# Kernel tuning notes

Hardware: AMD Instinct MI355X
Metric: run time of the kernel (lower is better)

## Reference

```python
import jax, jax.numpy as jnp
import numpy as np

B, T, N = 256, 512, 256
START, STOP = 254, 255


def setup_inputs() -> dict:
    key = jax.random.key(0)
    k1, k2, k3 = jax.random.split(key, 3)
    inputs = jax.random.normal(k1, (B, T, N), dtype=jnp.float32)
    transitions = jax.random.normal(k2, (N, N), dtype=jnp.float32)
    # sentinel rows/cols as in __init__
    transitions = transitions.at[START, :].set(-10000.0).at[:, STOP].set(-10000.0)
    tags = jax.random.randint(k3, (B, T), 0, N, dtype=jnp.int32)
    mask = jnp.ones((B, T), dtype=jnp.int32)
    return {"inputs": inputs, "transitions": transitions, "tags": tags, "mask": mask}


def _input_likelihood(inputs, transitions, fmask):
    # alpha[b, tag]: log-sum over paths ending at tag
    alpha0 = transitions[:, START][None, :] + inputs[:, 0, :]

    def step(alpha, xs):
        emit, m = xs  # emit: (B, N), m: (B,)
        # inner[b, next, prev] = alpha[b, prev] + (emit[b, next] + trans[next, prev]) * mask[b, i-1]
        inner = alpha[:, None, :] + (emit[:, :, None] + transitions[None, :, :]) * m[:, None, None]
        return jax.nn.logsumexp(inner, axis=-1), None

    xs = (jnp.swapaxes(inputs[:, 1:, :], 0, 1), jnp.swapaxes(fmask[:, :-1], 0, 1))
    alpha, _ = jax.lax.scan(step, alpha0, xs)
    stops = alpha + transitions[STOP][None, :]
    return jax.nn.logsumexp(stops, axis=-1)  # (B,)


def _joint_likelihood(inputs, transitions, tags, fmask):
    score = transitions[tags[:, 0], START]  # (B,)
    # transitions[next, prev] * mask[:, i+1], summed over steps
    trans_sc = transitions[tags[:, 1:], tags[:, :-1]] * fmask[:, 1:]
    # inputs[b, i, prev_tag] * mask[:, i]
    emit_sc = jnp.take_along_axis(inputs[:, :-1, :], tags[:, :-1, None], axis=2)[..., 0] * fmask[:, :-1]
    score = score + trans_sc.sum(axis=-1) + emit_sc.sum(axis=-1)
    last_idx = (fmask.sum(axis=-1) - 1.0).astype(jnp.int32)  # (B,)
    last_tags = jnp.take_along_axis(tags, last_idx[:, None], axis=1)[:, 0]
    last_input = jnp.take_along_axis(inputs[:, -1, :], last_tags[:, None], axis=1)[:, 0]
    return score + transitions[STOP, last_tags] + last_input * fmask[:, -1]


def reference(inputs, transitions, tags, mask):
    fmask = mask.astype(jnp.float32)
    log_denominator = _input_likelihood(inputs, transitions, fmask)
    log_numerator = _joint_likelihood(inputs, transitions, tags, fmask)
    return jnp.sum(log_numerator - log_denominator)
```

## Files before the change

### kernel.cpp

```cpp
#include <hip/hip_runtime.h>
#include <hip/hip_bf16.h>
#include <stdint.h>

#define B_    256
#define T_    512
#define N_    256
#define START_ 254
#define STOP_  255
#define GCOLS 16
#define NF    16
#define ND    32
#define LOG2E 1.4426950408889634f
#define LN2   0.6931471805599453f

#define WSB_OFF 65536
#define WCF_OFF 131072
#define WCB_OFF 131328

typedef __attribute__((ext_vector_type(4))) float floatx4;
typedef __attribute__((ext_vector_type(4))) unsigned int uintx4;
typedef __attribute__((ext_vector_type(8))) int v8i;

template<bool X> struct BC { static constexpr bool value = X; };

__device__ __forceinline__ void lds_barrier() {
    asm volatile("s_waitcnt lgkmcnt(0)\n\ts_barrier" ::: "memory");
}

__device__ __forceinline__ int pk_fp8x4(float a, float b, float c, float d) {
    int r = __builtin_amdgcn_cvt_pk_fp8_f32(a, b, 0, false);
    return __builtin_amdgcn_cvt_pk_fp8_f32(c, d, r, true);
}
__device__ __forceinline__ int pk_bf8x4(float a, float b, float c, float d) {
    int r = __builtin_amdgcn_cvt_pk_bf8_f32(a, b, 0, false);
    return __builtin_amdgcn_cvt_pk_bf8_f32(c, d, r, true);
}

struct DenomShared {
    alignas(16) char  V[2][4096];
    alignas(16) float mbuf[GCOLS * 36];
    alignas(16) float sbuf[GCOLS * 20];
    int flag;
};

template<bool ISF>
__device__ __forceinline__ void denom_path(
    DenomShared& sh, const float* __restrict__ inputs,
    const float* __restrict__ trans, const int* __restrict__ mask,
    float* __restrict__ ws, int blkLocal)
{
    const int tid = threadIdx.x;
    const int w = tid >> 6;
    const int l = tid & 63;
    const int q = l >> 4;
    const int b = l & 15;
    const int bg = blkLocal * GCOLS + b;
    const int j0 = 32 * w + 4 * q;
    const int S = ISF ? 256 : 255;
    const int scl = 0x7F7F7F7F;

    auto EIDX = [](int s) { return ISF ? s : (511 - s); };
    auto MIDX = [](int s) { return ISF ? (s - 1) : (511 - s); };

    int wa[2];
    #pragma unroll
    for (int mt = 0; mt < 2; ++mt)
        wa[mt] = ((((2 * w + mt) >> 3) * 2 + mt) << 10)
               + ((w & 3) << 8) + (b << 4) + (q << 2);
    const int rbase = l << 4;

    v8i afrag[2][2];
    #pragma unroll
    for (int mt = 0; mt < 2; ++mt) {
        const int row = 32 * w + 16 * mt + b;
        #pragma unroll
        for (int c = 0; c < 2; ++c) {
            v8i a;
            #pragma unroll
            for (int g8 = 0; g8 < 8; ++g8) {
                float e[4];
                if (ISF) {
                    floatx4 t = *(const floatx4*)(trans + row * N_ + c * 128 + q * 32 + 4 * g8);
                    #pragma unroll
                    for (int ii = 0; ii < 4; ++ii)
                        e[ii] = __builtin_amdgcn_exp2f(t[ii] * LOG2E);
                } else {
                    #pragma unroll
                    for (int ii = 0; ii < 4; ++ii) {
                        const int k = c * 128 + q * 32 + 4 * g8 + ii;
                        e[ii] = __builtin_amdgcn_exp2f(trans[k * N_ + row] * LOG2E);
                    }
                }
                a[g8] = pk_fp8x4(e[0], e[1], e[2], e[3]);
            }
            afrag[mt][c] = a;
        }
    }

    {
        const int* mrow = mask + blkLocal * GCOLS * T_;
        bool hd = false;
        #pragma unroll
        for (int i = 0; i < GCOLS * T_ / 512; ++i)
            hd |= (mrow[tid + 512 * i] == 0);
        if (tid == 0) sh.flag = 0;
        __syncthreads();
        if (__any(hd) && l == 0) atomicOr(&sh.flag, 1);
        __syncthreads();
    }
    const bool anyDead = (sh.flag != 0);

    const float* emitp = inputs + (size_t)bg * T_ * N_;
    const int*   maskp = mask + bg * T_;
    float C = 0.f;
    float u[2][4];

    if (ISF) {
        #pragma unroll
        for (int mt = 0; mt < 2; ++mt) {
            floatx4 em = *(const floatx4*)(emitp + j0 + 16 * mt);
            #pragma unroll
            for (int r = 0; r < 4; ++r) {
                const int j = j0 + 16 * mt + r;
                u[mt][r] = __builtin_amdgcn_exp2f((trans[j * N_ + START_] + em[r]) * LOG2E);
            }
        }
    } else {
        #pragma unroll
        for (int mt = 0; mt < 2; ++mt) {
            floatx4 st = *(const floatx4*)(trans + STOP_ * N_ + j0 + 16 * mt);
            #pragma unroll
            for (int r = 0; r < 4; ++r)
                u[mt][r] = __builtin_amdgcn_exp2f(st[r] * LOG2E);
        }
    }
    {
        float mx = u[0][0], sm = 0.f;
        #pragma unroll
        for (int mt = 0; mt < 2; ++mt)
            #pragma unroll
            for (int r = 0; r < 4; ++r) { mx = fmaxf(mx, u[mt][r]); sm += u[mt][r]; }
        sh.mbuf[b * 36 + w * 4 + q] = mx;
        sm += __shfl_xor(sm, 32, 64);
        if (l < 32) sh.sbuf[b * 20 + w * 2 + q] = sm;

        float xpi[2][4] = {{1.f,1.f,1.f,1.f},{1.f,1.f,1.f,1.f}};
        if (!ISF) {
            #pragma unroll
            for (int mt = 0; mt < 2; ++mt) {
                floatx4 e = *(const floatx4*)(emitp + (size_t)511 * N_ + j0 + 16 * mt);
                #pragma unroll
                for (int r = 0; r < 4; ++r)
                    xpi[mt][r] = __builtin_amdgcn_exp2f(e[r] * LOG2E);
            }
        }
        #pragma unroll
        for (int mt = 0; mt < 2; ++mt)
            *(int*)(sh.V[0] + wa[mt]) =
                pk_bf8x4(u[mt][0] * xpi[mt][0], u[mt][1] * xpi[mt][1],
                         u[mt][2] * xpi[mt][2], u[mt][3] * xpi[mt][3]);
    }

    auto run = [&](auto fastc) {
        constexpr bool FAST = decltype(fastc)::value;
        floatx4 ebuf[2][2];
        float   mrot[2] = {1.f, 1.f};
        ebuf[0][0] = *(const floatx4*)(emitp + (size_t)EIDX(1) * N_ + j0);
        ebuf[0][1] = *(const floatx4*)(emitp + (size_t)EIDX(1) * N_ + j0 + 16);
        ebuf[1][0] = *(const floatx4*)(emitp + (size_t)EIDX(2) * N_ + j0);
        ebuf[1][1] = *(const floatx4*)(emitp + (size_t)EIDX(2) * N_ + j0 + 16);
        if (!FAST) {
            mrot[0] = (float)maskp[MIDX(1)];
            mrot[1] = (float)maskp[MIDX(2)];
        }
        lds_barrier();

        auto body = [&](int s, int pr, int cur) {
            const int sp = (s + 2 <= S) ? s + 2 : S;
            floatx4 eC0 = *(const floatx4*)(emitp + (size_t)EIDX(sp) * N_ + j0);
            floatx4 eC1 = *(const floatx4*)(emitp + (size_t)EIDX(sp) * N_ + j0 + 16);
            float mC = 1.f;
            if (!FAST) mC = (float)maskp[MIDX(sp)];

            const char* vb = sh.V[pr];
            v8i bfrag[2];
            #pragma unroll
            for (int c = 0; c < 2; ++c) {
                uintx4 r0 = *(const uintx4*)(vb + (c << 11) + rbase);
                uintx4 r1 = *(const uintx4*)(vb + (c << 11) + 1024 + rbase);
                v8i bf;
                bf[0] = r0[0]; bf[1] = r0[1]; bf[2] = r0[2]; bf[3] = r0[3];
                bf[4] = r1[0]; bf[5] = r1[1]; bf[6] = r1[2]; bf[7] = r1[3];
                bfrag[c] = bf;
            }

            const float* mb = &sh.mbuf[b * 36];
            float cmax;
            {
                floatx4 mm[8];
                #pragma unroll
                for (int i = 0; i < 8; ++i) mm[i] = *(const floatx4*)(mb + 4 * i);
                floatx4 mv = mm[0];
                #pragma unroll
                for (int i = 1; i < 8; ++i)
                    #pragma unroll
                    for (int r = 0; r < 4; ++r) mv[r] = fmaxf(mv[r], mm[i][r]);
                cmax = fmaxf(fmaxf(mv[0], mv[1]), fmaxf(mv[2], mv[3]));
            }
            const uint32_t cb = __builtin_bit_cast(uint32_t, cmax);
            const int eb = (int)((cb >> 23) & 0xFFu);
            const float rs = __builtin_bit_cast(float, (uint32_t)(249 - eb) << 23);
            const float dCf = (float)(122 - eb);

            float xpv[2][4];
            #pragma unroll
            for (int r = 0; r < 4; ++r) {
                if (ISF) {
                    xpv[0][r] = __builtin_amdgcn_exp2f(fmaf(ebuf[cur][0][r], LOG2E, dCf));
                    xpv[1][r] = __builtin_amdgcn_exp2f(fmaf(ebuf[cur][1][r], LOG2E, dCf));
                } else {
                    xpv[0][r] = __builtin_amdgcn_exp2f(ebuf[cur][0][r] * LOG2E);
                    xpv[1][r] = __builtin_amdgcn_exp2f(ebuf[cur][1][r] * LOG2E);
                }
            }

            floatx4 a0 = {0.f,0.f,0.f,0.f}, a1 = {0.f,0.f,0.f,0.f};
            a0 = __builtin_amdgcn_mfma_scale_f32_16x16x128_f8f6f4(
                     afrag[0][0], bfrag[0], a0, 0, 1, 0, scl, 0, scl);
            a1 = __builtin_amdgcn_mfma_scale_f32_16x16x128_f8f6f4(
                     afrag[1][0], bfrag[0], a1, 0, 1, 0, scl, 0, scl);
            a0 = __builtin_amdgcn_mfma_scale_f32_16x16x128_f8f6f4(
                     afrag[0][1], bfrag[1], a0, 0, 1, 0, scl, 0, scl);
            a1 = __builtin_amdgcn_mfma_scale_f32_16x16x128_f8f6f4(
                     afrag[1][1], bfrag[1], a1, 0, 1, 0, scl, 0, scl);

            if (FAST) {
                #pragma unroll
                for (int r = 0; r < 4; ++r) {
                    if (ISF) {
                        u[0][r] = a0[r] * xpv[0][r];
                        u[1][r] = a1[r] * xpv[1][r];
                    } else {
                        u[0][r] = a0[r] * rs;
                        u[1][r] = a1[r] * rs;
                    }
                }
            } else {
                const bool live = (mrot[cur] != 0.f);
                float csv = 0.f;
                if (__any(!live)) {
                    const float* sb = &sh.sbuf[b * 20];
                    floatx4 s0 = *(const floatx4*)sb,       s1 = *(const floatx4*)(sb + 4);
                    floatx4 s2 = *(const floatx4*)(sb + 8), s3 = *(const floatx4*)(sb + 12);
                    csv = ((((s0[0] + s0[1]) + (s0[2] + s0[3])) +
                            ((s1[0] + s1[1]) + (s1[2] + s1[3]))) +
                           (((s2[0] + s2[1]) + (s2[2] + s2[3])) +
                            ((s3[0] + s3[1]) + (s3[2] + s3[3])))) * rs;
                }
                #pragma unroll
                for (int r = 0; r < 4; ++r) {
                    if (ISF) {
                        u[0][r] = live ? a0[r] * xpv[0][r] : csv;
                        u[1][r] = live ? a1[r] * xpv[1][r] : csv;
                    } else {
                        u[0][r] = live ? a0[r] * rs : csv;
                        u[1][r] = live ? a1[r] * rs : csv;
                    }
                }
            }
            C += (float)(eb - 122);

            {
                float mx = fmaxf(fmaxf(fmaxf(u[0][0], u[0][1]), fmaxf(u[0][2], u[0][3])),
                                 fmaxf(fmaxf(u[1][0], u[1][1]), fmaxf(u[1][2], u[1][3])));
                sh.mbuf[b * 36 + w * 4 + q] = mx;
                if (!FAST) {
                    float sm = ((u[0][0] + u[0][1]) + (u[0][2] + u[0][3]))
                             + ((u[1][0] + u[1][1]) + (u[1][2] + u[1][3]));
                    sm += __shfl_xor(sm, 32, 64);
                    if (l < 32) sh.sbuf[b * 20 + w * 2 + q] = sm;
                }
            }
            #pragma unroll
            for (int mt = 0; mt < 2; ++mt) {
                *(int*)(sh.V[pr ^ 1] + wa[mt]) = ISF
                    ? pk_bf8x4(u[mt][0], u[mt][1], u[mt][2], u[mt][3])
                    : pk_bf8x4(u[mt][0] * xpv[mt][0], u[mt][1] * xpv[mt][1],
                               u[mt][2] * xpv[mt][2], u[mt][3] * xpv[mt][3]);
            }
            lds_barrier();
            ebuf[cur][0] = eC0; ebuf[cur][1] = eC1;
            if (!FAST) mrot[cur] = mC;
        };

        #pragma unroll 1
        for (int g = 0; g < 127; ++g) {
            body(2 * g + 1, 0, 0);
            body(2 * g + 2, 1, 1);
        }
        if (ISF) { body(255, 0, 0); body(256, 1, 1); }
        else     { body(255, 0, 0); }
    };

    if (anyDead) run(BC<false>{});
    else         run(BC<true>{});

    float* wsV = ws + (ISF ? 0 : WSB_OFF);
    #pragma unroll
    for (int mt = 0; mt < 2; ++mt) {
        floatx4 vv = {u[mt][0], u[mt][1], u[mt][2], u[mt][3]};
        *(floatx4*)&wsV[(size_t)bg * N_ + j0 + 16 * mt] = vv;
    }
    if (tid < 16) {
        float* wsC = ws + (ISF ? WCF_OFF : WCB_OFF);
        wsC[blkLocal * GCOLS + tid] = C;
    }
}

__global__ __launch_bounds__(512, 2) void crf_main(
    const float* __restrict__ inputs, const float* __restrict__ trans,
    const int* __restrict__ tags, const int* __restrict__ mask,
    float* __restrict__ out, float* __restrict__ ws)
{
    __shared__ DenomShared sh;

    if (blockIdx.x >= ND) {
        float* nred = sh.sbuf;
        int*   nredi = (int*)(sh.sbuf + 8);
        const int bb = blockIdx.x - ND;
        const int t  = threadIdx.x;
        const int tg = tags[bb * T_ + t];
        const float fm = (float)mask[bb * T_ + t];
        float part = 0.f;
        if (t >= 1)      part += trans[tg * N_ + tags[bb * T_ + t - 1]] * fm;
        if (t <= T_ - 2) part += inputs[((size_t)bb * T_ + t) * N_ + tg] * fm;
        int ms = mask[bb * T_ + t];
        #pragma unroll
        for (int off = 1; off < 64; off <<= 1) {
            part += __shfl_xor(part, off, 64);
            ms   += __shfl_xor(ms, off, 64);
        }
        if ((t & 63) == 0) { nred[t >> 6] = part; nredi[t >> 6] = ms; }
        __syncthreads();
        if (t == 0) {
            float tot = 0.f; int mtot = 0;
            for (int i = 0; i < 8; ++i) { tot += nred[i]; mtot += nredi[i]; }
            tot += trans[tags[bb * T_] * N_ + START_];
            const int last = mtot - 1;
            const int lt = tags[bb * T_ + last];
            tot += trans[STOP_ * N_ + lt]
                 + inputs[((size_t)bb * T_ + (T_ - 1)) * N_ + lt]
                   * (float)mask[bb * T_ + T_ - 1];
            atomicAdd(out, tot);
        }
        return;
    }

    if (blockIdx.x < NF) denom_path<true>(sh, inputs, trans, mask, ws, blockIdx.x);
    else                 denom_path<false>(sh, inputs, trans, mask, ws, blockIdx.x - NF);
}

__global__ __launch_bounds__(256) void crf_combine(
    const float* __restrict__ ws, float* __restrict__ out)
{
    __shared__ float red[4];
    const int bb = blockIdx.x;
    const int t = threadIdx.x;
    float p = ws[(size_t)bb * N_ + t] * ws[WSB_OFF + (size_t)bb * N_ + t];
    #pragma unroll
    for (int off = 1; off < 64; off <<= 1) p += __shfl_xor(p, off, 64);
    if ((t & 63) == 0) red[t >> 6] = p;
    __syncthreads();
    if (t == 0) {
        const float tot = red[0] + red[1] + red[2] + red[3];
        const float denom = (ws[WCF_OFF + bb] + ws[WCB_OFF + bb]
                             + __builtin_amdgcn_logf(tot)) * LN2;
        atomicAdd(out, -denom);
    }
}

extern "C" void kernel_launch(void* const* d_in, const int* in_sizes, int n_in,
                              void* d_out, int out_size, void* d_ws, size_t ws_size,
                              hipStream_t stream) {
    const float* inputs = (const float*)d_in[0];
    const float* trans  = (const float*)d_in[1];
    const int*   tags   = (const int*)d_in[2];
    const int*   mask   = (const int*)d_in[3];
    float* out = (float*)d_out;
    float* ws  = (float*)d_ws;
    hipMemsetAsync(out, 0, sizeof(float), stream);
    crf_main<<<dim3(ND + B_), dim3(512), 0, stream>>>(inputs, trans, tags, mask, out, ws);
    crf_combine<<<dim3(B_), dim3(256), 0, stream>>>(ws, out);
}
```

Before: 341.0 us.

## Streamline serial CRF recurrence step: pointer-stepped prefetch, shuffle max, deferred exp

Reworks the per-timestep body of the forward/backward CRF recurrence. The running-max reduction now uses wave shuffles, so each step reads 8 floats from LDS instead of 32. Emission exponentials are computed one step ahead through a three-deep register rotation, and pointers are incremented rather than recomputing indices. The normalization exponent is accumulated as an integer and the forward scale is applied by multiplication instead of inside exp2. The numerator no longer uses one atomic per batch row; it goes to workspace, and the combine kernel handles 16 rows per block, which cuts atomics and blocks. The cost is more register pressure from the extra prefetch stage.

New measurement: 338.1 us. About the same (-0.9%).

```diff
diff --git a/kernel.cpp b/kernel.cpp
--- a/kernel.cpp
+++ b/kernel.cpp
@@ -16,6 +16,7 @@
 #define WSB_OFF 65536
 #define WCF_OFF 131072
 #define WCB_OFF 131328
+#define WNUM_OFF 131584
 
 typedef __attribute__((ext_vector_type(4))) float floatx4;
 typedef __attribute__((ext_vector_type(4))) unsigned int uintx4;
@@ -26,6 +27,9 @@
 __device__ __forceinline__ void lds_barrier() {
     asm volatile("s_waitcnt lgkmcnt(0)\n\ts_barrier" ::: "memory");
 }
+__device__ __forceinline__ float fmax3(float a, float b, float c) {
+    return fmaxf(fmaxf(a, b), c);
+}
 
 __device__ __forceinline__ int pk_fp8x4(float a, float b, float c, float d) {
     int r = __builtin_amdgcn_cvt_pk_fp8_f32(a, b, 0, false);
@@ -38,7 +42,7 @@
 
 struct DenomShared {
     alignas(16) char  V[2][4096];
-    alignas(16) float mbuf[GCOLS * 36];
+    alignas(16) float mbuf[GCOLS * 12];
     alignas(16) float sbuf[GCOLS * 20];
     int flag;
 };
@@ -112,7 +116,7 @@
 
     const float* emitp = inputs + (size_t)bg * T_ * N_;
     const int*   maskp = mask + bg * T_;
-    float C = 0.f;
+    int   Ci = 0;
     float u[2][4];
 
     if (ISF) {
@@ -135,12 +139,16 @@
         }
     }
     {
-        float mx = u[0][0], sm = 0.f;
+        float mx = fmaxf(fmax3(u[0][0], u[0][1], u[0][2]),
+                         fmax3(u[0][3], u[1][0], fmax3(u[1][1], u[1][2], u[1][3])));
+        float sm = 0.f;
         #pragma unroll
         for (int mt = 0; mt < 2; ++mt)
             #pragma unroll
-            for (int r = 0; r < 4; ++r) { mx = fmaxf(mx, u[mt][r]); sm += u[mt][r]; }
-        sh.mbuf[b * 36 + w * 4 + q] = mx;
+            for (int r = 0; r < 4; ++r) sm += u[mt][r];
+        mx = fmaxf(mx, __shfl_xor(mx, 16, 64));
+        mx = fmaxf(mx, __shfl_xor(mx, 32, 64));
+        if (l < 16) sh.mbuf[b * 12 + w] = mx;
         sm += __shfl_xor(sm, 32, 64);
         if (l < 32) sh.sbuf[b * 20 + w * 2 + q] = sm;
 
@@ -163,83 +171,94 @@
 
     auto run = [&](auto fastc) {
         constexpr bool FAST = decltype(fastc)::value;
-        floatx4 ebuf[2][2];
-        float   mrot[2] = {1.f, 1.f};
-        ebuf[0][0] = *(const floatx4*)(emitp + (size_t)EIDX(1) * N_ + j0);
-        ebuf[0][1] = *(const floatx4*)(emitp + (size_t)EIDX(1) * N_ + j0 + 16);
-        ebuf[1][0] = *(const floatx4*)(emitp + (size_t)EIDX(2) * N_ + j0);
-        ebuf[1][1] = *(const floatx4*)(emitp + (size_t)EIDX(2) * N_ + j0 + 16);
+        const long estep = ISF ? (long)N_ : -(long)N_;
+        const int  mstep = ISF ? 1 : -1;
+
+        floatx4 xc0, xc1;
+        floatx4 rbA0, rbA1;
+        floatx4 rbB0, rbB1;
+        const float* pe = emitp + (size_t)EIDX(1) * N_ + j0;
+        {
+            floatx4 e0 = *(const floatx4*)pe;
+            floatx4 e1 = *(const floatx4*)(pe + 16);
+            pe += estep;
+            rbA0 = *(const floatx4*)pe;
+            rbA1 = *(const floatx4*)(pe + 16);
+            pe += estep;
+            rbB0 = *(const floatx4*)pe;
+            rbB1 = *(const floatx4*)(pe + 16);
+            pe += estep;
+            #pragma unroll
+            for (int r = 0; r < 4; ++r) {
+                xc0[r] = __builtin_amdgcn_exp2f(e0[r] * LOG2E);
+                xc1[r] = __builtin_amdgcn_exp2f(e1[r] * LOG2E);
+            }
+        }
+        float mrot[2] = {1.f, 1.f};
+        const int* pm = maskp;
         if (!FAST) {
             mrot[0] = (float)maskp[MIDX(1)];
             mrot[1] = (float)maskp[MIDX(2)];
+            pm = maskp + MIDX(3);
         }
         lds_barrier();
 
-        auto body = [&](int s, int pr, int cur) {
-            const int sp = (s + 2 <= S) ? s + 2 : S;
-            floatx4 eC0 = *(const floatx4*)(emitp + (size_t)EIDX(sp) * N_ + j0);
-            floatx4 eC1 = *(const floatx4*)(emitp + (size_t)EIDX(sp) * N_ + j0 + 16);
+        auto body = [&](int pr, int cur) {
+            const char* vb = sh.V[pr];
+            uintx4 r00 = *(const uintx4*)(vb + rbase);
+            uintx4 r01 = *(const uintx4*)(vb + 1024 + rbase);
+            uintx4 r10 = *(const uintx4*)(vb + 2048 + rbase);
+            uintx4 r11 = *(const uintx4*)(vb + 3072 + rbase);
+            const float* mb = &sh.mbuf[b * 12];
+            floatx4 m0 = *(const floatx4*)mb;
+            floatx4 m1 = *(const floatx4*)(mb + 4);
+            floatx4 eC0 = *(const floatx4*)pe;
+            floatx4 eC1 = *(const floatx4*)(pe + 16);
             float mC = 1.f;
-            if (!FAST) mC = (float)maskp[MIDX(sp)];
-
-            const char* vb = sh.V[pr];
-            v8i bfrag[2];
-            #pragma unroll
-            for (int c = 0; c < 2; ++c) {
-                uintx4 r0 = *(const uintx4*)(vb + (c << 11) + rbase);
-                uintx4 r1 = *(const uintx4*)(vb + (c << 11) + 1024 + rbase);
-                v8i bf;
-                bf[0] = r0[0]; bf[1] = r0[1]; bf[2] = r0[2]; bf[3] = r0[3];
-                bf[4] = r1[0]; bf[5] = r1[1]; bf[6] = r1[2]; bf[7] = r1[3];
-                bfrag[c] = bf;
-            }
-
-            const float* mb = &sh.mbuf[b * 36];
-            float cmax;
-            {
-                floatx4 mm[8];
-                #pragma unroll
-                for (int i = 0; i < 8; ++i) mm[i] = *(const floatx4*)(mb + 4 * i);
-                floatx4 mv = mm[0];
-                #pragma unroll
-                for (int i = 1; i < 8; ++i)
-                    #pragma unroll
-                    for (int r = 0; r < 4; ++r) mv[r] = fmaxf(mv[r], mm[i][r]);
-                cmax = fmaxf(fmaxf(mv[0], mv[1]), fmaxf(mv[2], mv[3]));
-            }
+            if (!FAST) mC = (float)(*pm);
+
+            floatx4 xn0, xn1;
+            #pragma unroll
+            for (int r = 0; r < 4; ++r) {
+                xn0[r] = __builtin_amdgcn_exp2f(rbA0[r] * LOG2E);
+                xn1[r] = __builtin_amdgcn_exp2f(rbA1[r] * LOG2E);
+            }
+
+            floatx4 mv;
+            #pragma unroll
+            for (int r = 0; r < 4; ++r) mv[r] = fmaxf(m0[r], m1[r]);
+            const float cmax = fmax3(mv[0], mv[1], fmaxf(mv[2], mv[3]));
             const uint32_t cb = __builtin_bit_cast(uint32_t, cmax);
             const int eb = (int)((cb >> 23) & 0xFFu);
             const float rs = __builtin_bit_cast(float, (uint32_t)(249 - eb) << 23);
-            const float dCf = (float)(122 - eb);
-
-            float xpv[2][4];
-            #pragma unroll
-            for (int r = 0; r < 4; ++r) {
-                if (ISF) {
-                    xpv[0][r] = __builtin_amdgcn_exp2f(fmaf(ebuf[cur][0][r], LOG2E, dCf));
-                    xpv[1][r] = __builtin_amdgcn_exp2f(fmaf(ebuf[cur][1][r], LOG2E, dCf));
-                } else {
-                    xpv[0][r] = __builtin_amdgcn_exp2f(ebuf[cur][0][r] * LOG2E);
-                    xpv[1][r] = __builtin_amdgcn_exp2f(ebuf[cur][1][r] * LOG2E);
-                }
-            }
+            Ci += eb;
+
+            floatx4 rx0, rx1;
+            if (ISF) {
+                #pragma unroll
+                for (int r = 0; r < 4; ++r) { rx0[r] = xc0[r] * rs; rx1[r] = xc1[r] * rs; }
+            }
+
+            union { v8i v; struct { uintx4 lo, hi; } p; } bf0, bf1;
+            bf0.p.lo = r00; bf0.p.hi = r01;
+            bf1.p.lo = r10; bf1.p.hi = r11;
 
             floatx4 a0 = {0.f,0.f,0.f,0.f}, a1 = {0.f,0.f,0.f,0.f};
             a0 = __builtin_amdgcn_mfma_scale_f32_16x16x128_f8f6f4(
-                     afrag[0][0], bfrag[0], a0, 0, 1, 0, scl, 0, scl);
+                     afrag[0][0], bf0.v, a0, 0, 1, 0, scl, 0, scl);
             a1 = __builtin_amdgcn_mfma_scale_f32_16x16x128_f8f6f4(
-                     afrag[1][0], bfrag[0], a1, 0, 1, 0, scl, 0, scl);
+                     afrag[1][0], bf0.v, a1, 0, 1, 0, scl, 0, scl);
             a0 = __builtin_amdgcn_mfma_scale_f32_16x16x128_f8f6f4(
-                     afrag[0][1], bfrag[1], a0, 0, 1, 0, scl, 0, scl);
+                     afrag[0][1], bf1.v, a0, 0, 1, 0, scl, 0, scl);
             a1 = __builtin_amdgcn_mfma_scale_f32_16x16x128_f8f6f4(
-                     afrag[1][1], bfrag[1], a1, 0, 1, 0, scl, 0, scl);
+                     afrag[1][1], bf1.v, a1, 0, 1, 0, scl, 0, scl);
 
             if (FAST) {
                 #pragma unroll
                 for (int r = 0; r < 4; ++r) {
                     if (ISF) {
-                        u[0][r] = a0[r] * xpv[0][r];
-                        u[1][r] = a1[r] * xpv[1][r];
+                        u[0][r] = a0[r] * rx0[r];
+                        u[1][r] = a1[r] * rx1[r];
                     } else {
                         u[0][r] = a0[r] * rs;
                         u[1][r] = a1[r] * rs;
@@ -260,20 +279,22 @@
                 #pragma unroll
                 for (int r = 0; r < 4; ++r) {
                     if (ISF) {
-                        u[0][r] = live ? a0[r] * xpv[0][r] : csv;
-                        u[1][r] = live ? a1[r] * xpv[1][r] : csv;
+                        u[0][r] = live ? a0[r] * rx0[r] : csv;
+                        u[1][r] = live ? a1[r] * rx1[r] : csv;
                     } else {
                         u[0][r] = live ? a0[r] * rs : csv;
                         u[1][r] = live ? a1[r] * rs : csv;
                     }
                 }
             }
-            C += (float)(eb - 122);
 
             {
-                float mx = fmaxf(fmaxf(fmaxf(u[0][0], u[0][1]), fmaxf(u[0][2], u[0][3])),
-                                 fmaxf(fmaxf(u[1][0], u[1][1]), fmaxf(u[1][2], u[1][3])));
-                sh.mbuf[b * 36 + w * 4 + q] = mx;
+                float mx = fmaxf(fmax3(u[0][0], u[0][1], u[0][2]),
+                                 fmax3(u[0][3], u[1][0],
+                                       fmax3(u[1][1], u[1][2], u[1][3])));
+                mx = fmaxf(mx, __shfl_xor(mx, 16, 64));
+                mx = fmaxf(mx, __shfl_xor(mx, 32, 64));
+                if (l < 16) sh.mbuf[b * 12 + w] = mx;
                 if (!FAST) {
                     float sm = ((u[0][0] + u[0][1]) + (u[0][2] + u[0][3]))
                              + ((u[1][0] + u[1][1]) + (u[1][2] + u[1][3]));
@@ -281,25 +302,31 @@
                     if (l < 32) sh.sbuf[b * 20 + w * 2 + q] = sm;
                 }
             }
-            #pragma unroll
-            for (int mt = 0; mt < 2; ++mt) {
-                *(int*)(sh.V[pr ^ 1] + wa[mt]) = ISF
-                    ? pk_bf8x4(u[mt][0], u[mt][1], u[mt][2], u[mt][3])
-                    : pk_bf8x4(u[mt][0] * xpv[mt][0], u[mt][1] * xpv[mt][1],
-                               u[mt][2] * xpv[mt][2], u[mt][3] * xpv[mt][3]);
+            if (ISF) {
+                *(int*)(sh.V[pr ^ 1] + wa[0]) = pk_bf8x4(u[0][0], u[0][1], u[0][2], u[0][3]);
+                *(int*)(sh.V[pr ^ 1] + wa[1]) = pk_bf8x4(u[1][0], u[1][1], u[1][2], u[1][3]);
+            } else {
+                *(int*)(sh.V[pr ^ 1] + wa[0]) =
+                    pk_bf8x4(u[0][0] * xc0[0], u[0][1] * xc0[1],
+                             u[0][2] * xc0[2], u[0][3] * xc0[3]);
+                *(int*)(sh.V[pr ^ 1] + wa[1]) =
+                    pk_bf8x4(u[1][0] * xc1[0], u[1][1] * xc1[1],
+                             u[1][2] * xc1[2], u[1][3] * xc1[3]);
             }
             lds_barrier();
-            ebuf[cur][0] = eC0; ebuf[cur][1] = eC1;
-            if (!FAST) mrot[cur] = mC;
+            xc0 = xn0; xc1 = xn1;
+            rbA0 = rbB0; rbA1 = rbB1;
+            rbB0 = eC0;  rbB1 = eC1;
+            pe += estep;
+            if (!FAST) { mrot[cur] = mC; pm += mstep; }
         };
 
         #pragma unroll 1
-        for (int g = 0; g < 127; ++g) {
-            body(2 * g + 1, 0, 0);
-            body(2 * g + 2, 1, 1);
-        }
-        if (ISF) { body(255, 0, 0); body(256, 1, 1); }
-        else     { body(255, 0, 0); }
+        for (int g = 0; g < S / 2; ++g) {
+            body(0, 0);
+            body(1, 1);
+        }
+        if (S & 1) body(0, 0);
     };
 
     if (anyDead) run(BC<false>{});
@@ -313,7 +340,7 @@
     }
     if (tid < 16) {
         float* wsC = ws + (ISF ? WCF_OFF : WCB_OFF);
-        wsC[blkLocal * GCOLS + tid] = C;
+        wsC[blkLocal * GCOLS + tid] = (float)(Ci - 122 * S);
     }
 }
 
@@ -351,7 +378,7 @@
             tot += trans[STOP_ * N_ + lt]
                  + inputs[((size_t)bb * T_ + (T_ - 1)) * N_ + lt]
                    * (float)mask[bb * T_ + T_ - 1];
-            atomicAdd(out, tot);
+            ws[WNUM_OFF + bb] = tot;
         }
         return;
     }
@@ -364,19 +391,28 @@
     const float* __restrict__ ws, float* __restrict__ out)
 {
     __shared__ float red[4];
-    const int bb = blockIdx.x;
     const int t = threadIdx.x;
-    float p = ws[(size_t)bb * N_ + t] * ws[WSB_OFF + (size_t)bb * N_ + t];
-    #pragma unroll
-    for (int off = 1; off < 64; off <<= 1) p += __shfl_xor(p, off, 64);
-    if ((t & 63) == 0) red[t >> 6] = p;
+    const int w = t >> 6, l = t & 63;
+    float acc = 0.f;
+    #pragma unroll 1
+    for (int i = 0; i < 4; ++i) {
+        const int bb = blockIdx.x * GCOLS + w * 4 + i;
+        const float* pa = ws + (size_t)bb * N_;
+        const float* pb = ws + WSB_OFF + (size_t)bb * N_;
+        floatx4 va = *(const floatx4*)(pa + 4 * l);
+        floatx4 vb = *(const floatx4*)(pb + 4 * l);
+        float p = va[0] * vb[0] + va[1] * vb[1] + va[2] * vb[2] + va[3] * vb[3];
+        #pragma unroll
+        for (int off = 1; off < 64; off <<= 1) p += __shfl_xor(p, off, 64);
+        if (l == 0) {
+            const float denom = (ws[WCF_OFF + bb] + ws[WCB_OFF + bb]
+                                 + __builtin_amdgcn_logf(p)) * LN2;
+            acc += ws[WNUM_OFF + bb] - denom;
+        }
+    }
+    if (l == 0) red[w] = acc;
     __syncthreads();
-    if (t == 0) {
-        const float tot = red[0] + red[1] + red[2] + red[3];
-        const float denom = (ws[WCF_OFF + bb] + ws[WCB_OFF + bb]
-                             + __builtin_amdgcn_logf(tot)) * LN2;
-        atomicAdd(out, -denom);
-    }
+    if (t == 0) atomicAdd(out, red[0] + red[1] + red[2] + red[3]);
 }
 
 extern "C" void kernel_launch(void* const* d_in, const int* in_sizes, int n_in,
@@ -390,5 +426,5 @@
     float* ws  = (float*)d_ws;
     hipMemsetAsync(out, 0, sizeof(float), stream);
     crf_main<<<dim3(ND + B_), dim3(512), 0, stream>>>(inputs, trans, tags, mask, out, ws);
-    crf_combine<<<dim3(B_), dim3(256), 0, stream>>>(ws, out);
-}
+    crf_combine<<<dim3(B_ / GCOLS), dim3(256), 0, stream>>>(ws, out);
+}
```
